# Optimization experiments

Hardware: AMD Instinct MI355X
Metric: run time of the kernel (lower is better)

The kernel has to match this reference:

```python
import math
import jax, jax.numpy as jnp
import numpy as np

D_MODEL, D_HEAD, BLOCK, B, N = 1024, 128, 2048, 4, 2048
# mode_gate('wake') blend weights (omega_lang, omega_grav)
OMEGA_LANG, OMEGA_GRAV = 0.7, 0.3


def setup_inputs() -> dict:
    key = jax.random.key(0)
    kx, kq, kk, kv, kl = jax.random.split(key, 5)
    x = jax.random.normal(kx, (B, N, D_MODEL), dtype=jnp.float32)
    # nn.Linear(d_model, d_head, bias=False) -> store as [d_model, d_head] for x @ W
    s = 1.0 / math.sqrt(D_MODEL)
    Wq = jax.random.uniform(kq, (D_MODEL, D_HEAD), jnp.float32, -s, s)
    Wk = jax.random.uniform(kk, (D_MODEL, D_HEAD), jnp.float32, -s, s)
    Wv = jax.random.uniform(kv, (D_MODEL, D_HEAD), jnp.float32, -s, s)
    # L_grav = eye*0.3 + randn*0.05
    L_grav = jnp.eye(D_HEAD, dtype=jnp.float32) * 0.3 \
        + jax.random.normal(kl, (D_HEAD, D_HEAD), dtype=jnp.float32) * 0.05
    return {"x": x, "Wq": Wq, "Wk": Wk, "Wv": Wv, "L_grav": L_grav}


def reference(x, Wq, Wk, Wv, L_grav):
    b, n, _ = x.shape
    d_head = Wq.shape[1]
    q = x @ Wq          # [b, n, d]
    k = x @ Wk          # [b, n, d]
    v = x @ Wv          # [b, n, d]
    mask = jnp.tril(jnp.ones((n, n), dtype=bool))  # causal, broadcast over batch

    # lang_attention: scaled dot-product with causal softmax
    scores = jnp.einsum('bqd,bkd->bqk', q, k) / math.sqrt(d_head)
    scores = jnp.where(mask, scores, -jnp.inf)
    a_lang = jax.nn.softmax(scores, axis=-1)       # [b, n, n]

    # grav_attention: Gaussian kernel on Mahalanobis-transformed keys y = k @ L_grav,
    # sigma = sqrt(d_head); masked + row-normalized (non-softmax).
    y = k @ L_grav                                  # [b, n, d]
    sq = jnp.sum(y * y, axis=-1)                    # [b, n]
    gram = jnp.einsum('bqd,bkd->bqk', y, y)         # [b, n, n]
    dist2 = jnp.maximum(sq[:, :, None] + sq[:, None, :] - 2.0 * gram, 0.0)
    kern = jnp.exp(-dist2 / (2.0 * d_head))         # sigma^2 = d_head
    kern = jnp.where(mask, kern, 0.0)
    a_grav = kern / (jnp.sum(kern, axis=-1, keepdims=True) + 1e-8)

    a = OMEGA_LANG * a_lang + OMEGA_GRAV * a_grav   # mode='wake' gate blend
    return a @ v                                    # [b, n, d_head]
```

## Files before the change

kernel.cpp:

```cpp
#include <hip/hip_runtime.h>
#include <hip/hip_bf16.h>
#include <math.h>

typedef __attribute__((ext_vector_type(8))) short short8;
typedef __attribute__((ext_vector_type(4))) short s16x4;
typedef __attribute__((ext_vector_type(4))) float f32x4;

#define SEQ 2048
#define DH 128

__device__ __forceinline__ short f2bf(float f) {
    union { float f; unsigned u; } v; v.f = f;
    unsigned r = v.u + 0x7fffu + ((v.u >> 16) & 1u);
    return (short)(r >> 16);
}
__device__ __forceinline__ float bf2f(short s) {
    union { unsigned u; float f; } v; v.u = ((unsigned)(unsigned short)s) << 16;
    return v.f;
}

__device__ __forceinline__ void gll16(const void* g, void* l) {
    __builtin_amdgcn_global_load_lds(
        (const __attribute__((address_space(1))) unsigned int*)g,
        (__attribute__((address_space(3))) unsigned int*)l, 16, 0, 0);
}

__global__ __launch_bounds__(256) void wt_kernel(
    const float* __restrict__ Wq, const float* __restrict__ Wk, const float* __restrict__ Wv,
    short* __restrict__ Wt2)
{
    const int t = threadIdx.x;
    const int m  = blockIdx.x >> 4;
    const int ks = blockIdx.x & 15;
    const float* W = m == 0 ? Wq : (m == 1 ? Wk : Wv);
    short* dst = Wt2 + ((size_t)(m * 16 + ks) * 1024) * 8;
    #pragma unroll
    for (int j = 0; j < 4; j++) {
        const int idx = t * 4 + j;
        const int ctile = idx >> 7;
        const int kc = (idx >> 6) & 1;
        const int gg = (idx >> 4) & 3;
        const int cc = idx & 15;
        const int col = ctile * 16 + cc;
        const int kb = ks * 64 + kc * 32 + gg * 8;
        short8 h;
        #pragma unroll
        for (int e = 0; e < 8; e++) h[e] = f2bf(W[(size_t)(kb + e) * 128 + col]);
        *(short8*)&dst[idx * 8] = h;
    }
}

__global__ __launch_bounds__(256) void proj_kernel(
    const float* __restrict__ x, const short* __restrict__ Wt2,
    short* __restrict__ Qh, short* __restrict__ Kh, short* __restrict__ Vh)
{
    __shared__ short Xs[2048];
    __shared__ short Ws[8192];
    const int t = threadIdx.x;
    const int w = t >> 6, l = t & 63;
    const int c = l & 15, g = l >> 4;
    const int bid = blockIdx.x;
    const int m = bid % 3;
    const int row0 = (bid / 3) * 32;
    const short* Wm = Wt2 + (size_t)m * 16 * 1024 * 8;

    const int xr = t >> 3;
    const int xk = (t & 7) * 8;
    const int xIdx = ((xr >> 4) * 2 + (xk >> 5)) * 64 + ((xk >> 3) & 3) * 16 + (xr & 15);

    const int rt = w & 1;
    const int ct4 = (w >> 1) * 4;
    f32x4 acc[4];
    #pragma unroll
    for (int nt = 0; nt < 4; nt++) acc[nt] = (f32x4)0.f;

    for (int ks = 0; ks < 16; ks++) {
        __syncthreads();
        const short* wsrc = Wm + ((size_t)ks * 1024 + w * 256 + l) * 8;
        #pragma unroll
        for (int j = 0; j < 4; j++)
            gll16(wsrc + j * 64 * 8, (void*)&Ws[(w * 256 + j * 64) * 8]);
        {
            const float* xp = &x[(size_t)(row0 + xr) * 1024 + ks * 64 + xk];
            const float4 a = *(const float4*)xp;
            const float4 b = *(const float4*)(xp + 4);
            short8 h;
            h[0] = f2bf(a.x); h[1] = f2bf(a.y); h[2] = f2bf(a.z); h[3] = f2bf(a.w);
            h[4] = f2bf(b.x); h[5] = f2bf(b.y); h[6] = f2bf(b.z); h[7] = f2bf(b.w);
            *(short8*)&Xs[xIdx * 8] = h;
        }
        __syncthreads();
        #pragma unroll
        for (int kc = 0; kc < 2; kc++) {
            const short8 af = *(const short8*)&Xs[((rt * 2 + kc) * 64 + l) * 8];
            #pragma unroll
            for (int nt = 0; nt < 4; nt++) {
                const short8 bf = *(const short8*)&Ws[(((ct4 + nt) * 2 + kc) * 64 + l) * 8];
                acc[nt] = __builtin_amdgcn_mfma_f32_16x16x32_bf16(af, bf, acc[nt], 0, 0, 0);
            }
        }
    }
    short* Out = m == 0 ? Qh : (m == 1 ? Kh : Vh);
    #pragma unroll
    for (int nt = 0; nt < 4; nt++)
        #pragma unroll
        for (int r = 0; r < 4; r++)
            Out[(size_t)(row0 + rt * 16 + 4 * g + r) * 128 + (ct4 + nt) * 16 + c] = f2bf(acc[nt][r]);
}

__global__ __launch_bounds__(256) void y_kernel(
    const short* __restrict__ Kh, const float* __restrict__ L,
    short* __restrict__ Yh, float* __restrict__ SQ)
{
    __shared__ float Ls[128 * 128];
    __shared__ short Ks[16][128];
    const int t = threadIdx.x;
    const int row0 = blockIdx.x * 16;
    #pragma unroll
    for (int j = 0; j < 16; j++) {
        int lin = t + j * 256;
        ((float4*)Ls)[lin] = ((const float4*)L)[lin];
    }
    {
        int r = t >> 4, ch = t & 15;
        *(short8*)&Ks[r][ch * 8] = *(const short8*)&Kh[(size_t)(row0 + r) * 128 + ch * 8];
    }
    __syncthreads();
    const int rl = t >> 4, c4 = (t & 15) * 4;
    float acc[8] = {};
    for (int d = 0; d < 128; d++) {
        const float kd = bf2f(Ks[rl][d]);
        const float4 l0 = *(const float4*)&Ls[d * 128 + c4];
        const float4 l1 = *(const float4*)&Ls[d * 128 + c4 + 64];
        acc[0] += kd * l0.x; acc[1] += kd * l0.y; acc[2] += kd * l0.z; acc[3] += kd * l0.w;
        acc[4] += kd * l1.x; acc[5] += kd * l1.y; acc[6] += kd * l1.z; acc[7] += kd * l1.w;
    }
    const int row = row0 + rl;
    s16x4 h0, h1;
    float s = 0.f;
    #pragma unroll
    for (int j = 0; j < 4; j++) {
        short h = f2bf(acc[j]);     float rv = bf2f(h); s += rv * rv; h0[j] = h;
        short g = f2bf(acc[j + 4]); float gv = bf2f(g); s += gv * gv; h1[j] = g;
    }
    *(s16x4*)&Yh[(size_t)row * 128 + c4]      = h0;
    *(s16x4*)&Yh[(size_t)row * 128 + c4 + 64] = h1;
    for (int off = 1; off < 16; off <<= 1) s += __shfl_xor(s, off);
    if ((t & 15) == 0) SQ[row] = s;
}

__global__ __launch_bounds__(256) void vt_kernel(
    const short* __restrict__ Vh, short* __restrict__ Vt)
{
    __shared__ short Ls[64][72];
    const int t = threadIdx.x;
    const int b  = blockIdx.x >> 6;
    const int nb = (blockIdx.x >> 1) & 31;
    const int db = blockIdx.x & 1;
    const int n0 = nb * 64, d0 = db * 64;
    const short* Vb = Vh + (size_t)b * SEQ * 128;
    short* Vtb = Vt + (size_t)b * 128 * SEQ;
    #pragma unroll
    for (int i = 0; i < 2; i++) {
        int row = (t >> 3) + 32 * i;
        int ch = t & 7;
        *(short8*)&Ls[row][ch * 8] = *(const short8*)&Vb[(size_t)(n0 + row) * 128 + d0 + ch * 8];
    }
    __syncthreads();
    #pragma unroll
    for (int i = 0; i < 2; i++) {
        int dd = (t >> 3) + 32 * i;
        int nc = t & 7;
        short8 v;
        #pragma unroll
        for (int j = 0; j < 8; j++) v[j] = Ls[nc * 8 + j][dd];
        *(short8*)&Vtb[(size_t)(d0 + dd) * SEQ + n0 + nc * 8] = v;
    }
}

__global__ __launch_bounds__(256, 2) void attn_kernel(
    const short* __restrict__ Qh, const short* __restrict__ Kh,
    const short* __restrict__ Yh, const short* __restrict__ Vt,
    const float* __restrict__ SQv,
    float* __restrict__ OL, float* __restrict__ OG,
    float* __restrict__ LS, float* __restrict__ GS)
{
    __shared__ __align__(16) short Bs[2][8192];
    __shared__ __align__(16) short Vs[2][8192];
    __shared__ __align__(16) short P[4 * 2 * 512];
    __shared__ float Rs[32];
    float* Obuf = (float*)&Bs[0][0];

    const int t = threadIdx.x;
    const int w = t >> 6, l = t & 63;
    const int c = l & 15, g = l >> 4;
    const int qh = w & 1, kh = w >> 1;
    const int wbase = t & 192;
    const int bid = blockIdx.x;
    const int b = bid & 3;
    const int grav = (bid >> 2) & 1;
    const int qt = 63 - (bid >> 3);
    const int q0 = qt * 32;
    const int nkt = (qt + 2) >> 1;

    const size_t boff = (size_t)b * SEQ * 128;
    const short* Ab = (grav ? Yh : Qh) + boff;
    const short* Bb = (grav ? Yh : Kh) + boff;
    const short* Vb = Vt + boff;
    const float* SQb = SQv + b * SEQ;

    const float CL = 0.12751743f;
    const float CG = -0.0056355275f;

    const short* bsrc[4];
    const short* vsrc[4];
    #pragma unroll
    for (int j = 0; j < 4; j++) {
        const int u = j * 256 + t;
        bsrc[j] = Bb + (size_t)(u & 63) * 128 + (u >> 6) * 8;
        vsrc[j] = Vb + (size_t)(u & 127) * SEQ + (u >> 7) * 8;
    }

    short8 qf[4];
    #pragma unroll
    for (int kc = 0; kc < 4; kc++)
        qf[kc] = *(const short8*)&Ab[(size_t)(q0 + qh * 16 + c) * 128 + kc * 32 + 8 * g];
    float sqq[4];
    if (grav) {
        #pragma unroll
        for (int r = 0; r < 4; r++)
            sqq[r] = SQb[q0 + qh * 16 + 4 * g + r];
    }

    f32x4 acc[8];
    #pragma unroll
    for (int dt = 0; dt < 8; dt++) acc[dt] = (f32x4)0.f;
    float rsum[4] = {};

    #pragma unroll
    for (int j = 0; j < 4; j++) gll16(bsrc[j], (void*)&Bs[0][(j * 256 + wbase) * 8]);
    #pragma unroll
    for (int j = 0; j < 4; j++) gll16(vsrc[j], (void*)&Vs[0][(j * 256 + wbase) * 8]);

    int cur = 0, pb = 0;
    for (int ti = 0; ti < nkt; ti++, cur ^= 1, pb ^= 1) {
        const int k0 = ti * 64;
        __syncthreads();
        if (ti + 1 < nkt) {
            const int kn = k0 + 64;
            #pragma unroll
            for (int j = 0; j < 4; j++)
                gll16(bsrc[j] + (size_t)kn * 128, (void*)&Bs[cur ^ 1][(j * 256 + wbase) * 8]);
            #pragma unroll
            for (int j = 0; j < 4; j++)
                gll16(vsrc[j] + kn, (void*)&Vs[cur ^ 1][(j * 256 + wbase) * 8]);
        }

        short* Pp = P + (w * 2 + pb) * 512;

        #pragma unroll
        for (int kt = 0; kt < 2; kt++) {
            f32x4 sc = (f32x4)0.f;
            #pragma unroll
            for (int kc = 0; kc < 4; kc++) {
                const short8 bf = *(const short8*)
                    &Bs[cur][((kc * 4 + g) * 64 + kh * 32 + kt * 16 + c) * 8];
                sc = __builtin_amdgcn_mfma_f32_16x16x32_bf16(qf[kc], bf, sc, 0, 0, 0);
            }
            const int key = k0 + kh * 32 + kt * 16 + c;
            const float sqkv = grav ? SQb[key] : 0.f;
            #pragma unroll
            for (int r = 0; r < 4; r++) {
                const int qrow = q0 + qh * 16 + 4 * g + r;
                float p = 0.f;
                if (key <= qrow) {
                    if (grav) {
                        float d2 = sqq[r] + sqkv - 2.f * sc[r];
                        d2 = fmaxf(d2, 0.f);
                        p = __builtin_amdgcn_exp2f(d2 * CG);
                    } else {
                        p = __builtin_amdgcn_exp2f(sc[r] * CL);
                    }
                }
                const short ph = f2bf(p);
                rsum[r] += bf2f(ph);
                const int row = 4 * g + r;
                Pp[row * 32 + ((kt * 16 + c) ^ (g << 3))] = ph;
            }
        }

        const short8 pf = *(const short8*)&Pp[c * 32 + 8 * (g ^ ((c >> 2) & 3))];
        #pragma unroll
        for (int dt = 0; dt < 8; dt++) {
            const short8 vf = *(const short8*)
                &Vs[cur][((kh * 4 + g) * 128 + dt * 16 + c) * 8];
            acc[dt] = __builtin_amdgcn_mfma_f32_16x16x32_bf16(pf, vf, acc[dt], 0, 0, 0);
        }
    }

    __syncthreads();
    for (int i = t; i < 32 * 132; i += 256) Obuf[i] = 0.f;
    if (t < 32) Rs[t] = 0.f;
    __syncthreads();

    #pragma unroll
    for (int dt = 0; dt < 8; dt++)
        #pragma unroll
        for (int r = 0; r < 4; r++)
            atomicAdd(&Obuf[(qh * 16 + 4 * g + r) * 132 + dt * 16 + c], acc[dt][r]);

    #pragma unroll
    for (int r = 0; r < 4; r++) {
        float v = rsum[r];
        v += __shfl_xor(v, 1); v += __shfl_xor(v, 2);
        v += __shfl_xor(v, 4); v += __shfl_xor(v, 8);
        rsum[r] = v;
    }
    if (c == 0) {
        #pragma unroll
        for (int r = 0; r < 4; r++)
            atomicAdd(&Rs[qh * 16 + 4 * g + r], rsum[r]);
    }
    __syncthreads();

    float* Op = (grav ? OG : OL) + boff + (size_t)q0 * 128;
    #pragma unroll
    for (int i = 0; i < 4; i++) {
        const int v = t + 256 * i;
        const int row = v >> 5, c4 = (v & 31) * 4;
        *(float4*)&Op[row * 128 + c4] = *(const float4*)&Obuf[row * 132 + c4];
    }
    if (t < 32) (grav ? GS : LS)[b * SEQ + q0 + t] = Rs[t];
}

__global__ __launch_bounds__(256) void finalize_kernel(
    float* __restrict__ out, const float* __restrict__ OG,
    const float* __restrict__ LS, const float* __restrict__ GS)
{
    const int i4 = blockIdx.x * 256 + threadIdx.x;
    float4 o = ((float4*)out)[i4];
    const float4 gv = ((const float4*)OG)[i4];
    const int row = i4 >> 5;
    const float wl = 0.7f / LS[row];
    const float wg = 0.3f / (GS[row] + 1e-8f);
    o.x = o.x * wl + gv.x * wg;
    o.y = o.y * wl + gv.y * wg;
    o.z = o.z * wl + gv.z * wg;
    o.w = o.w * wl + gv.w * wg;
    ((float4*)out)[i4] = o;
}

extern "C" void kernel_launch(void* const* d_in, const int* in_sizes, int n_in,
                              void* d_out, int out_size, void* d_ws, size_t ws_size,
                              hipStream_t stream) {
    const float* x  = (const float*)d_in[0];
    const float* Wq = (const float*)d_in[1];
    const float* Wk = (const float*)d_in[2];
    const float* Wv = (const float*)d_in[3];
    const float* Lg = (const float*)d_in[4];

    char* ws = (char*)d_ws;
    short* Qh  = (short*)(ws + 0);
    short* Kh  = (short*)(ws + 2097152);
    short* Vh  = (short*)(ws + 4194304);
    short* Yh  = (short*)(ws + 6291456);
    short* Vt  = (short*)(ws + 8388608);
    short* Wt2 = (short*)(ws + 10485760);
    float* SQv = (float*)(ws + 11272192);
    float* LS  = (float*)(ws + 11304960);
    float* GS  = (float*)(ws + 11337728);
    float* OG  = (float*)(ws + 11370496);
    float* OL  = (float*)d_out;

    wt_kernel<<<48, 256, 0, stream>>>(Wq, Wk, Wv, Wt2);
    proj_kernel<<<768, 256, 0, stream>>>(x, Wt2, Qh, Kh, Vh);
    y_kernel<<<512, 256, 0, stream>>>(Kh, Lg, Yh, SQv);
    vt_kernel<<<256, 256, 0, stream>>>(Vh, Vt);
    attn_kernel<<<512, 256, 0, stream>>>(Qh, Kh, Yh, Vt, SQv, OL, OG, LS, GS);
    finalize_kernel<<<1024, 256, 0, stream>>>((float*)d_out, OG, LS, GS);
}
```

Baseline: 140.7 us.

## Pre-tile Q/K/Y/V into MFMA fragment layout and balance causal attention work

Projection, y and transpose kernels now write Q, K, Y and V in a tiled 64-row fragment layout, so attention tiles load as contiguous 16 KB blocks. The attention kernel pairs query tile jp with tile 63-jp so every block does a similar amount of causal work. The key tiles are split across two blocks by parity, and their partial results are merged with global float atomics into buffers zeroed by added memsets. This evens out load across blocks and simplifies global loads, at the cost of extra memsets, heavy global atomic traffic and nondeterministic summation order.

```diff
diff --git a/kernel.cpp b/kernel.cpp
--- a/kernel.cpp
+++ b/kernel.cpp
@@ -8,6 +8,7 @@
 
 #define SEQ 2048
 #define DH 128
+
 
 __device__ __forceinline__ short f2bf(float f) {
     union { float f; unsigned u; } v; v.f = f;
@@ -104,8 +105,15 @@
     #pragma unroll
     for (int nt = 0; nt < 4; nt++)
         #pragma unroll
-        for (int r = 0; r < 4; r++)
-            Out[(size_t)(row0 + rt * 16 + 4 * g + r) * 128 + (ct4 + nt) * 16 + c] = f2bf(acc[nt][r]);
+        for (int r = 0; r < 4; r++) {
+            const int R = row0 + rt * 16 + 4 * g + r;
+            const int col = (ct4 + nt) * 16 + c;
+            const short hv = f2bf(acc[nt][r]);
+            if (m == 2)
+                Out[(size_t)R * 128 + col] = hv;
+            else
+                Out[(size_t)(R >> 6) * 8192 + ((col >> 3) * 64 + (R & 63)) * 8 + (col & 7)] = hv;
+        }
 }
 
 __global__ __launch_bounds__(256) void y_kernel(
@@ -123,7 +131,9 @@
     }
     {
         int r = t >> 4, ch = t & 15;
-        *(short8*)&Ks[r][ch * 8] = *(const short8*)&Kh[(size_t)(row0 + r) * 128 + ch * 8];
+        const int R = row0 + r;
+        *(short8*)&Ks[r][ch * 8] =
+            *(const short8*)&Kh[(size_t)(R >> 6) * 8192 + (ch * 64 + (R & 63)) * 8];
     }
     __syncthreads();
     const int rl = t >> 4, c4 = (t & 15) * 4;
@@ -135,7 +145,7 @@
         acc[0] += kd * l0.x; acc[1] += kd * l0.y; acc[2] += kd * l0.z; acc[3] += kd * l0.w;
         acc[4] += kd * l1.x; acc[5] += kd * l1.y; acc[6] += kd * l1.z; acc[7] += kd * l1.w;
     }
-    const int row = row0 + rl;
+    const int R = row0 + rl;
     s16x4 h0, h1;
     float s = 0.f;
     #pragma unroll
@@ -143,14 +153,15 @@
         short h = f2bf(acc[j]);     float rv = bf2f(h); s += rv * rv; h0[j] = h;
         short g = f2bf(acc[j + 4]); float gv = bf2f(g); s += gv * gv; h1[j] = g;
     }
-    *(s16x4*)&Yh[(size_t)row * 128 + c4]      = h0;
-    *(s16x4*)&Yh[(size_t)row * 128 + c4 + 64] = h1;
+    const size_t base = (size_t)(R >> 6) * 8192 + (size_t)(R & 63) * 8;
+    *(s16x4*)&Yh[base + (c4 >> 3) * 512 + (c4 & 7)] = h0;
+    *(s16x4*)&Yh[base + ((c4 + 64) >> 3) * 512 + (c4 & 7)] = h1;
     for (int off = 1; off < 16; off <<= 1) s += __shfl_xor(s, off);
-    if ((t & 15) == 0) SQ[row] = s;
+    if ((t & 15) == 0) SQ[R] = s;
 }
 
 __global__ __launch_bounds__(256) void vt_kernel(
-    const short* __restrict__ Vh, short* __restrict__ Vt)
+    const short* __restrict__ Vh, short* __restrict__ Vf)
 {
     __shared__ short Ls[64][72];
     const int t = threadIdx.x;
@@ -159,7 +170,7 @@
     const int db = blockIdx.x & 1;
     const int n0 = nb * 64, d0 = db * 64;
     const short* Vb = Vh + (size_t)b * SEQ * 128;
-    short* Vtb = Vt + (size_t)b * 128 * SEQ;
+    short* Vfb = Vf + (size_t)b * SEQ * 128;
     #pragma unroll
     for (int i = 0; i < 2; i++) {
         int row = (t >> 3) + 32 * i;
@@ -174,13 +185,13 @@
         short8 v;
         #pragma unroll
         for (int j = 0; j < 8; j++) v[j] = Ls[nc * 8 + j][dd];
-        *(short8*)&Vtb[(size_t)(d0 + dd) * SEQ + n0 + nc * 8] = v;
+        *(short8*)&Vfb[(size_t)(n0 >> 6) * 8192 + (nc * 128 + d0 + dd) * 8] = v;
     }
 }
 
 __global__ __launch_bounds__(256, 2) void attn_kernel(
-    const short* __restrict__ Qh, const short* __restrict__ Kh,
-    const short* __restrict__ Yh, const short* __restrict__ Vt,
+    const short* __restrict__ Qf, const short* __restrict__ Kf,
+    const short* __restrict__ Yf, const short* __restrict__ Vf,
     const float* __restrict__ SQv,
     float* __restrict__ OL, float* __restrict__ OG,
     float* __restrict__ LS, float* __restrict__ GS)
@@ -199,138 +210,145 @@
     const int bid = blockIdx.x;
     const int b = bid & 3;
     const int grav = (bid >> 2) & 1;
-    const int qt = 63 - (bid >> 3);
-    const int q0 = qt * 32;
-    const int nkt = (qt + 2) >> 1;
-
-    const size_t boff = (size_t)b * SEQ * 128;
-    const short* Ab = (grav ? Yh : Qh) + boff;
-    const short* Bb = (grav ? Yh : Kh) + boff;
-    const short* Vb = Vt + boff;
+    const int s = (bid >> 3) & 1;
+    const int jp = bid >> 4;
+
+    const size_t fb = (size_t)b * SEQ * 128;
+    const short* Ap = (grav ? Yf : Qf) + fb;
+    const short* Bp = (grav ? Yf : Kf) + fb;
+    const short* Vp = Vf + fb;
     const float* SQb = SQv + b * SEQ;
 
     const float CL = 0.12751743f;
     const float CG = -0.0056355275f;
 
-    const short* bsrc[4];
-    const short* vsrc[4];
-    #pragma unroll
-    for (int j = 0; j < 4; j++) {
-        const int u = j * 256 + t;
-        bsrc[j] = Bb + (size_t)(u & 63) * 128 + (u >> 6) * 8;
-        vsrc[j] = Vb + (size_t)(u & 127) * SEQ + (u >> 7) * 8;
-    }
-
-    short8 qf[4];
-    #pragma unroll
-    for (int kc = 0; kc < 4; kc++)
-        qf[kc] = *(const short8*)&Ab[(size_t)(q0 + qh * 16 + c) * 128 + kc * 32 + 8 * g];
-    float sqq[4];
-    if (grav) {
-        #pragma unroll
-        for (int r = 0; r < 4; r++)
-            sqq[r] = SQb[q0 + qh * 16 + 4 * g + r];
-    }
-
-    f32x4 acc[8];
-    #pragma unroll
-    for (int dt = 0; dt < 8; dt++) acc[dt] = (f32x4)0.f;
-    float rsum[4] = {};
-
-    #pragma unroll
-    for (int j = 0; j < 4; j++) gll16(bsrc[j], (void*)&Bs[0][(j * 256 + wbase) * 8]);
-    #pragma unroll
-    for (int j = 0; j < 4; j++) gll16(vsrc[j], (void*)&Vs[0][(j * 256 + wbase) * 8]);
-
-    int cur = 0, pb = 0;
-    for (int ti = 0; ti < nkt; ti++, cur ^= 1, pb ^= 1) {
-        const int k0 = ti * 64;
-        __syncthreads();
-        if (ti + 1 < nkt) {
-            const int kn = k0 + 64;
+    for (int m = 0; m < 2; m++) {
+        const int qt = m ? 63 - jp : jp;
+        const int q0 = qt * 32;
+        const int nkt = (qt + 2) >> 1;
+
+        __syncthreads();
+
+        short8 qf[4];
+        const size_t qtb = (size_t)(qt >> 1) * 8192;
+        const int qlocal = (qt & 1) * 32 + qh * 16 + c;
+        #pragma unroll
+        for (int kc = 0; kc < 4; kc++)
+            qf[kc] = *(const short8*)&Ap[qtb + ((kc * 4 + g) * 64 + qlocal) * 8];
+
+        float sqq[4];
+        if (grav) {
             #pragma unroll
-            for (int j = 0; j < 4; j++)
-                gll16(bsrc[j] + (size_t)kn * 128, (void*)&Bs[cur ^ 1][(j * 256 + wbase) * 8]);
-            #pragma unroll
-            for (int j = 0; j < 4; j++)
-                gll16(vsrc[j] + kn, (void*)&Vs[cur ^ 1][(j * 256 + wbase) * 8]);
-        }
-
-        short* Pp = P + (w * 2 + pb) * 512;
-
-        #pragma unroll
-        for (int kt = 0; kt < 2; kt++) {
-            f32x4 sc = (f32x4)0.f;
-            #pragma unroll
-            for (int kc = 0; kc < 4; kc++) {
-                const short8 bf = *(const short8*)
-                    &Bs[cur][((kc * 4 + g) * 64 + kh * 32 + kt * 16 + c) * 8];
-                sc = __builtin_amdgcn_mfma_f32_16x16x32_bf16(qf[kc], bf, sc, 0, 0, 0);
+            for (int r = 0; r < 4; r++)
+                sqq[r] = SQb[q0 + qh * 16 + 4 * g + r];
+        }
+
+        f32x4 acc[8];
+        #pragma unroll
+        for (int dt = 0; dt < 8; dt++) acc[dt] = (f32x4)0.f;
+        float rsum[4] = {};
+
+        if (s < nkt) {
+            {
+                const short* bs0 = Bp + (size_t)s * 8192;
+                const short* vs0 = Vp + (size_t)s * 8192;
+                #pragma unroll
+                for (int j = 0; j < 4; j++)
+                    gll16(bs0 + (j * 256 + t) * 8, (void*)&Bs[0][(j * 256 + wbase) * 8]);
+                #pragma unroll
+                for (int j = 0; j < 4; j++)
+                    gll16(vs0 + (j * 256 + t) * 8, (void*)&Vs[0][(j * 256 + wbase) * 8]);
             }
-            const int key = k0 + kh * 32 + kt * 16 + c;
-            const float sqkv = grav ? SQb[key] : 0.f;
-            #pragma unroll
-            for (int r = 0; r < 4; r++) {
-                const int qrow = q0 + qh * 16 + 4 * g + r;
-                float p = 0.f;
-                if (key <= qrow) {
-                    if (grav) {
-                        float d2 = sqq[r] + sqkv - 2.f * sc[r];
-                        d2 = fmaxf(d2, 0.f);
-                        p = __builtin_amdgcn_exp2f(d2 * CG);
-                    } else {
-                        p = __builtin_amdgcn_exp2f(sc[r] * CL);
+            int cur = 0, pb = 0;
+            for (int tt = s; tt < nkt; tt += 2, cur ^= 1, pb ^= 1) {
+                __syncthreads();
+                if (tt + 2 < nkt) {
+                    const short* bsn = Bp + (size_t)(tt + 2) * 8192;
+                    const short* vsn = Vp + (size_t)(tt + 2) * 8192;
+                    #pragma unroll
+                    for (int j = 0; j < 4; j++)
+                        gll16(bsn + (j * 256 + t) * 8, (void*)&Bs[cur ^ 1][(j * 256 + wbase) * 8]);
+                    #pragma unroll
+                    for (int j = 0; j < 4; j++)
+                        gll16(vsn + (j * 256 + t) * 8, (void*)&Vs[cur ^ 1][(j * 256 + wbase) * 8]);
+                }
+                const int k0 = tt * 64;
+                short* Pp = P + (w * 2 + pb) * 512;
+
+                #pragma unroll
+                for (int kt = 0; kt < 2; kt++) {
+                    f32x4 sc = (f32x4)0.f;
+                    #pragma unroll
+                    for (int kc = 0; kc < 4; kc++) {
+                        const short8 bf = *(const short8*)
+                            &Bs[cur][((kc * 4 + g) * 64 + kh * 32 + kt * 16 + c) * 8];
+                        sc = __builtin_amdgcn_mfma_f32_16x16x32_bf16(qf[kc], bf, sc, 0, 0, 0);
+                    }
+                    const int key = k0 + kh * 32 + kt * 16 + c;
+                    const float sqkv = grav ? SQb[key] : 0.f;
+                    #pragma unroll
+                    for (int r = 0; r < 4; r++) {
+                        const int qrow = q0 + qh * 16 + 4 * g + r;
+                        float p = 0.f;
+                        if (key <= qrow) {
+                            if (grav) {
+                                float d2 = sqq[r] + sqkv - 2.f * sc[r];
+                                d2 = fmaxf(d2, 0.f);
+                                p = __builtin_amdgcn_exp2f(d2 * CG);
+                            } else {
+                                p = __builtin_amdgcn_exp2f(sc[r] * CL);
+                            }
+                        }
+                        const short ph = f2bf(p);
+                        rsum[r] += bf2f(ph);
+                        const int row = 4 * g + r;
+                        Pp[row * 32 + ((kt * 16 + c) ^ (g << 3))] = ph;
                     }
                 }
-                const short ph = f2bf(p);
-                rsum[r] += bf2f(ph);
-                const int row = 4 * g + r;
-                Pp[row * 32 + ((kt * 16 + c) ^ (g << 3))] = ph;
+
+                const short8 pf = *(const short8*)&Pp[c * 32 + 8 * (g ^ ((c >> 2) & 3))];
+                #pragma unroll
+                for (int dt = 0; dt < 8; dt++) {
+                    const short8 vf = *(const short8*)
+                        &Vs[cur][((kh * 4 + g) * 128 + dt * 16 + c) * 8];
+                    acc[dt] = __builtin_amdgcn_mfma_f32_16x16x32_bf16(pf, vf, acc[dt], 0, 0, 0);
+                }
             }
         }
 
-        const short8 pf = *(const short8*)&Pp[c * 32 + 8 * (g ^ ((c >> 2) & 3))];
-        #pragma unroll
-        for (int dt = 0; dt < 8; dt++) {
-            const short8 vf = *(const short8*)
-                &Vs[cur][((kh * 4 + g) * 128 + dt * 16 + c) * 8];
-            acc[dt] = __builtin_amdgcn_mfma_f32_16x16x32_bf16(pf, vf, acc[dt], 0, 0, 0);
-        }
-    }
-
-    __syncthreads();
-    for (int i = t; i < 32 * 132; i += 256) Obuf[i] = 0.f;
-    if (t < 32) Rs[t] = 0.f;
-    __syncthreads();
-
-    #pragma unroll
-    for (int dt = 0; dt < 8; dt++)
-        #pragma unroll
-        for (int r = 0; r < 4; r++)
-            atomicAdd(&Obuf[(qh * 16 + 4 * g + r) * 132 + dt * 16 + c], acc[dt][r]);
-
-    #pragma unroll
-    for (int r = 0; r < 4; r++) {
-        float v = rsum[r];
-        v += __shfl_xor(v, 1); v += __shfl_xor(v, 2);
-        v += __shfl_xor(v, 4); v += __shfl_xor(v, 8);
-        rsum[r] = v;
-    }
-    if (c == 0) {
-        #pragma unroll
-        for (int r = 0; r < 4; r++)
-            atomicAdd(&Rs[qh * 16 + 4 * g + r], rsum[r]);
-    }
-    __syncthreads();
-
-    float* Op = (grav ? OG : OL) + boff + (size_t)q0 * 128;
-    #pragma unroll
-    for (int i = 0; i < 4; i++) {
-        const int v = t + 256 * i;
-        const int row = v >> 5, c4 = (v & 31) * 4;
-        *(float4*)&Op[row * 128 + c4] = *(const float4*)&Obuf[row * 132 + c4];
-    }
-    if (t < 32) (grav ? GS : LS)[b * SEQ + q0 + t] = Rs[t];
+        __syncthreads();
+        for (int i = t; i < 32 * 132; i += 256) Obuf[i] = 0.f;
+        if (t < 32) Rs[t] = 0.f;
+        __syncthreads();
+
+        #pragma unroll
+        for (int dt = 0; dt < 8; dt++)
+            #pragma unroll
+            for (int r = 0; r < 4; r++)
+                atomicAdd(&Obuf[(qh * 16 + 4 * g + r) * 132 + dt * 16 + c], acc[dt][r]);
+
+        #pragma unroll
+        for (int r = 0; r < 4; r++) {
+            float v = rsum[r];
+            v += __shfl_xor(v, 1); v += __shfl_xor(v, 2);
+            v += __shfl_xor(v, 4); v += __shfl_xor(v, 8);
+            rsum[r] = v;
+        }
+        if (c == 0) {
+            #pragma unroll
+            for (int r = 0; r < 4; r++)
+                atomicAdd(&Rs[qh * 16 + 4 * g + r], rsum[r]);
+        }
+        __syncthreads();
+
+        float* Op = (grav ? OG : OL) + fb + (size_t)q0 * 128;
+        #pragma unroll
+        for (int i = 0; i < 16; i++) {
+            const int v2 = t + 256 * i;
+            atomicAdd(&Op[v2], Obuf[(v2 >> 7) * 132 + (v2 & 127)]);
+        }
+        if (t < 32) atomicAdd(&(grav ? GS : LS)[b * SEQ + q0 + t], Rs[t]);
+    }
 }
 
 __global__ __launch_bounds__(256) void finalize_kernel(
@@ -364,7 +382,7 @@
     short* Kh  = (short*)(ws + 2097152);
     short* Vh  = (short*)(ws + 4194304);
     short* Yh  = (short*)(ws + 6291456);
-    short* Vt  = (short*)(ws + 8388608);
+    short* Vf  = (short*)(ws + 8388608);
     short* Wt2 = (short*)(ws + 10485760);
     float* SQv = (float*)(ws + 11272192);
     float* LS  = (float*)(ws + 11304960);
@@ -372,10 +390,14 @@
     float* OG  = (float*)(ws + 11370496);
     float* OL  = (float*)d_out;
 
+    hipMemsetAsync(d_out, 0, 4194304, stream);
+    hipMemsetAsync((void*)LS, 0, 65536, stream);
+    hipMemsetAsync((void*)OG, 0, 4194304, stream);
+
     wt_kernel<<<48, 256, 0, stream>>>(Wq, Wk, Wv, Wt2);
     proj_kernel<<<768, 256, 0, stream>>>(x, Wt2, Qh, Kh, Vh);
     y_kernel<<<512, 256, 0, stream>>>(Kh, Lg, Yh, SQv);
-    vt_kernel<<<256, 256, 0, stream>>>(Vh, Vt);
-    attn_kernel<<<512, 256, 0, stream>>>(Qh, Kh, Yh, Vt, SQv, OL, OG, LS, GS);
+    vt_kernel<<<256, 256, 0, stream>>>(Vh, Vf);
+    attn_kernel<<<512, 256, 0, stream>>>(Qh, Kh, Yh, Vf, SQv, OL, OG, LS, GS);
     finalize_kernel<<<1024, 256, 0, stream>>>((float*)d_out, OG, LS, GS);
 }
```

After: 127.9 us. 1.1x faster.
